# Kernel optimization log

Measured on AMD Instinct MI355X. Metric: run time of the kernel, lower is better.

The kernel has to match this reference:

```python
import jax, jax.numpy as jnp
import numpy as np

N_NODES = 50000
N_EDGES = 800000
IN_FEATS = 64
HID_FEATS = 64


def setup_inputs() -> dict:
    key = jax.random.key(0)
    ks = jax.random.split(key, 5)
    x = jax.random.normal(ks[0], (N_NODES, IN_FEATS), dtype=jnp.float32)
    src = jax.random.randint(ks[1], (N_EDGES,), 0, N_NODES)
    dst = jax.random.randint(ks[2], (N_EDGES,), 0, N_NODES)
    # GraphConv parameters (Glorot-ish init, bias zeros as in dgl defaults)
    W1 = jax.random.normal(ks[3], (IN_FEATS, HID_FEATS), dtype=jnp.float32) / np.sqrt(IN_FEATS)
    b1 = jnp.zeros((HID_FEATS,), dtype=jnp.float32)
    W2 = jax.random.normal(ks[4], (HID_FEATS, IN_FEATS), dtype=jnp.float32) / np.sqrt(HID_FEATS)
    b2 = jnp.zeros((IN_FEATS,), dtype=jnp.float32)
    return {"x": x, "src": src, "dst": dst, "W1": W1, "b1": b1, "W2": W2, "b2": b2}


def _graph_conv(x, src, dst, W, b, n_nodes):
    """dgl GraphConv with norm='both': D_dst^{-1/2} A D_src^{-1/2} X W + b."""
    ones = jnp.ones((src.shape[0],), dtype=x.dtype)
    deg_out = jax.ops.segment_sum(ones, src, num_segments=n_nodes)
    deg_in = jax.ops.segment_sum(ones, dst, num_segments=n_nodes)
    norm_out = jnp.where(deg_out > 0, jax.lax.rsqrt(jnp.maximum(deg_out, 1.0)), 0.0)
    norm_in = jnp.where(deg_in > 0, jax.lax.rsqrt(jnp.maximum(deg_in, 1.0)), 0.0)
    h = x * norm_out[:, None]                                  # [N, F] scaled by src norm
    agg = jax.ops.segment_sum(h[src], dst, num_segments=n_nodes)  # gather over edges + scatter-add
    return (agg * norm_in[:, None]) @ W + b


def reference(x, src, dst, W1, b1, W2, b2):
    n, d = x.shape
    # dHdx: conv -> tanh -> conv
    y = jnp.tanh(_graph_conv(x, src, dst, W1, b1, n))
    y = _graph_conv(y, src, dst, W2, b2, n)
    # J = cat([I[d//2:], -I[:d//2]])  -> symplectic [[0, I], [-I, 0]]
    I = jnp.eye(d, dtype=x.dtype)
    J = jnp.concatenate([I[d // 2:], -I[: d // 2]], axis=0)
    # get_D is undefined in the source module; treated as zero dissipation term.
    return y @ J.T
```

## Files before the change

### kernel.cpp

```cpp
#include <hip/hip_runtime.h>
#include <hip/hip_bf16.h>
#include <math.h>

#define N_NODES 50000
#define N_EDGES 800000
#define F 64
#define NPAD 50048
#define NBLK ((N_NODES + 255) / 256)

#define P_HIST 256
#define CHUNK (N_EDGES / P_HIST)
#define WORDS8 12500
#define RBLK8 ((WORDS8 + 255) / 256)
#define RSPLIT 4
#define WR (WORDS8 / RSPLIT)
#define HBLK (P_HIST * RSPLIT)

#define TW 20
#define RV3BLK (WORDS8 / TW)
#define TS 260

#define LROW 36
#define LBLK ((N_NODES + 31) / 32)

typedef short short8 __attribute__((ext_vector_type(8)));
typedef float f32x4 __attribute__((ext_vector_type(4)));

__device__ inline unsigned short f2bf(float f) {
    unsigned u = __float_as_uint(f);
    unsigned r = (u + 0x7fffu + ((u >> 16) & 1u)) >> 16;
    return (unsigned short)r;
}
__device__ inline float bf2f(unsigned v) { return __uint_as_float(v << 16); }
__device__ inline float bf2f_hi(unsigned v) { return __uint_as_float(v & 0xffff0000u); }

__device__ inline unsigned wave_incl_scan(unsigned v, int lane) {
    #pragma unroll
    for (int d = 1; d < 64; d <<= 1) {
        unsigned u = __shfl_up(v, d, 64);
        if (lane >= d) v += u;
    }
    return v;
}


__global__ __launch_bounds__(256) void hist2_kernel(
    const int* __restrict__ src, const int* __restrict__ dst,
    unsigned* __restrict__ histd, unsigned* __restrict__ hists)
{
    __shared__ unsigned ldd[WR];
    __shared__ unsigned lsd[WR];
    int bid = blockIdx.x, t = threadIdx.x;
    int p = bid >> 2, r = bid & 3;
    int e0 = p * CHUNK;
    unsigned wbase = (unsigned)(r * WR);
    for (int i = t; i < WR; i += 256) { ldd[i] = 0; lsd[i] = 0; }
    __syncthreads();
    for (int i = t; i < CHUNK; i += 256) {
        int d = dst[e0 + i];
        int s = src[e0 + i];
        unsigned wd = ((unsigned)d >> 2) - wbase;
        unsigned ws = ((unsigned)s >> 2) - wbase;
        if (wd < WR) atomicAdd(&ldd[wd], 1u << ((d & 3) * 8));
        if (ws < WR) atomicAdd(&lsd[ws], 1u << ((s & 3) * 8));
    }
    __syncthreads();
    unsigned* outd = histd + (size_t)p * WORDS8 + r * WR;
    unsigned* outs = hists + (size_t)p * WORDS8 + r * WR;
    for (int i = t; i < WR; i += 256) { outd[i] = ldd[i]; outs[i] = lsd[i]; }
}

__global__ __launch_bounds__(256) void reduce_v3_kernel(
    unsigned* __restrict__ histd, const unsigned* __restrict__ hists,
    float* __restrict__ norm_in, float* __restrict__ norm_out,
    int* __restrict__ row_off, unsigned* __restrict__ wordsum)
{
    __shared__ unsigned lds[TW * TS];
    int t = threadIdx.x, b = blockIdx.x;
    int lane = t & 63, ww = t >> 6;
    int w0 = b * TW;

    {
        uint4* gp = (uint4*)(histd + (size_t)t * WORDS8 + w0);
        #pragma unroll
        for (int i = 0; i < TW / 4; ++i) {
            uint4 v = gp[i];
            lds[(i * 4 + 0) * TS + t] = v.x;
            lds[(i * 4 + 1) * TS + t] = v.y;
            lds[(i * 4 + 2) * TS + t] = v.z;
            lds[(i * 4 + 3) * TS + t] = v.w;
        }
    }
    __syncthreads();
    #pragma unroll
    for (int k = 0; k < TW / 4; ++k) {
        int lw = ww + k * 4;
        uint4 h = *(uint4*)(lds + lw * TS + 4 * lane);
        unsigned lsum = h.x + h.y + h.z + h.w;
        unsigned inc = lsum;
        #pragma unroll
        for (int d = 1; d < 64; d <<= 1) {
            unsigned u = __shfl_up(inc, d, 64);
            if (lane >= d) inc += u;
        }
        unsigned run = inc - lsum;
        uint4 o;
        o.x = run; run += h.x;
        o.y = run; run += h.y;
        o.z = run; run += h.z;
        o.w = run;
        *(uint4*)(lds + lw * TS + 4 * lane) = o;
        unsigned total = __shfl(inc, 63, 64);
        if (lane == 0) {
            int w = w0 + lw;
            unsigned d0 = total & 255u, d1 = (total >> 8) & 255u;
            unsigned d2 = (total >> 16) & 255u, d3 = total >> 24;
            norm_in[4 * w]     = d0 ? rsqrtf((float)d0) : 0.f;
            norm_in[4 * w + 1] = d1 ? rsqrtf((float)d1) : 0.f;
            norm_in[4 * w + 2] = d2 ? rsqrtf((float)d2) : 0.f;
            norm_in[4 * w + 3] = d3 ? rsqrtf((float)d3) : 0.f;
            int4 r;
            r.x = 0; r.y = (int)d0; r.z = (int)(d0 + d1); r.w = (int)(d0 + d1 + d2);
            *(int4*)(row_off + 4 * w) = r;
            wordsum[w] = d0 + d1 + d2 + d3;
        }
    }
    __syncthreads();
    {
        uint4* gp = (uint4*)(histd + (size_t)t * WORDS8 + w0);
        #pragma unroll
        for (int i = 0; i < TW / 4; ++i) {
            uint4 v;
            v.x = lds[(i * 4 + 0) * TS + t];
            v.y = lds[(i * 4 + 1) * TS + t];
            v.z = lds[(i * 4 + 2) * TS + t];
            v.w = lds[(i * 4 + 3) * TS + t];
            gp[i] = v;
        }
    }
    __syncthreads();

    {
        const uint4* gp = (const uint4*)(hists + (size_t)t * WORDS8 + w0);
        #pragma unroll
        for (int i = 0; i < TW / 4; ++i) {
            uint4 v = gp[i];
            lds[(i * 4 + 0) * TS + t] = v.x;
            lds[(i * 4 + 1) * TS + t] = v.y;
            lds[(i * 4 + 2) * TS + t] = v.z;
            lds[(i * 4 + 3) * TS + t] = v.w;
        }
    }
    __syncthreads();
    #pragma unroll
    for (int k = 0; k < TW / 4; ++k) {
        int lw = ww + k * 4;
        uint4 h = *(uint4*)(lds + lw * TS + 4 * lane);
        unsigned s = h.x + h.y + h.z + h.w;
        #pragma unroll
        for (int d = 1; d < 64; d <<= 1) s += __shfl_xor(s, d, 64);
        if (lane == 0) {
            int w = w0 + lw;
            unsigned t0 = s & 255u, t1 = (s >> 8) & 255u;
            unsigned t2 = (s >> 16) & 255u, t3 = s >> 24;
            norm_out[4 * w]     = t0 ? rsqrtf((float)t0) : 0.f;
            norm_out[4 * w + 1] = t1 ? rsqrtf((float)t1) : 0.f;
            norm_out[4 * w + 2] = t2 ? rsqrtf((float)t2) : 0.f;
            norm_out[4 * w + 3] = t3 ? rsqrtf((float)t3) : 0.f;
        }
    }
}

__global__ __launch_bounds__(256) void scanw_kernel(
    const unsigned* __restrict__ wordsum, int* __restrict__ row_off,
    unsigned* __restrict__ blockSums)
{
    __shared__ unsigned wsum[4];
    int t = threadIdx.x, b = blockIdx.x;
    int w = b * 256 + t;
    unsigned v = (w < WORDS8) ? wordsum[w] : 0u;
    int lane = t & 63, wid = t >> 6;
    unsigned inc = wave_incl_scan(v, lane);
    if (lane == 63) wsum[wid] = inc;
    __syncthreads();
    if (t == 0) {
        unsigned acc = 0;
        #pragma unroll
        for (int q = 0; q < 4; ++q) { unsigned x = wsum[q]; wsum[q] = acc; acc += x; }
    }
    __syncthreads();
    unsigned excl = inc - v + wsum[wid];
    if (w < WORDS8) {
        int4 r = *(int4*)(row_off + 4 * w);
        r.x += (int)excl; r.y += (int)excl; r.z += (int)excl; r.w += (int)excl;
        *(int4*)(row_off + 4 * w) = r;
    }
    if (t == 255) blockSums[b] = excl + v;
}

__global__ __launch_bounds__(256) void scan_fin_kernel(
    const unsigned* __restrict__ blockSums, int* __restrict__ row_off)
{
    __shared__ unsigned off_s;
    int t = threadIdx.x, b = blockIdx.x;
    if (t < 64) {
        unsigned v = (t < b) ? blockSums[t] : 0u;
        #pragma unroll
        for (int d = 1; d < 64; d <<= 1) v += __shfl_xor(v, d, 64);
        if (t == 0) off_s = v;
    }
    __syncthreads();
    int off = (int)off_s;
    int w = b * 256 + t;
    if (w < WORDS8) {
        int4 r = *(int4*)(row_off + 4 * w);
        r.x += off; r.y += off; r.z += off; r.w += off;
        *(int4*)(row_off + 4 * w) = r;
    }
    if (w == 0) row_off[N_NODES] = N_EDGES;
}

__global__ __launch_bounds__(256) void scatter2_kernel(
    const int* __restrict__ src, const int* __restrict__ dst,
    const int* __restrict__ row_off, const unsigned* __restrict__ histd,
    int* __restrict__ csr_src)
{
    __shared__ unsigned rk[WR];
    __shared__ unsigned pf[WR];
    int bid = blockIdx.x, t = threadIdx.x;
    int p = bid >> 2, r = bid & 3;
    int e0 = p * CHUNK;
    unsigned wbase = (unsigned)(r * WR);
    const unsigned* pref = histd + (size_t)p * WORDS8 + r * WR;
    for (int i = t; i < WR; i += 256) { rk[i] = 0; pf[i] = pref[i]; }
    __syncthreads();
    for (int i = t; i < CHUNK; i += 256) {
        int d = dst[e0 + i];
        int s = src[e0 + i];
        unsigned wd = ((unsigned)d >> 2) - wbase;
        if (wd < WR) {
            int sh = (d & 3) * 8;
            unsigned old = atomicAdd(&rk[wd], 1u << sh);
            unsigned rank = (old >> sh) & 255u;
            unsigned pre  = (pf[wd] >> sh) & 255u;
            csr_src[row_off[d] + (int)(pre + rank)] = s;
        }
    }
}


__global__ __launch_bounds__(256) void degrees_kernel(
    const int* __restrict__ src, const int* __restrict__ dst,
    unsigned* __restrict__ deg_out_u, unsigned* __restrict__ deg_in_u)
{
    int e = blockIdx.x * 256 + threadIdx.x;
    if (e < N_EDGES) {
        atomicAdd(&deg_out_u[src[e]], 1u);
        atomicAdd(&deg_in_u[dst[e]], 1u);
    }
}

__global__ __launch_bounds__(256) void fb_scan_a_kernel(
    const unsigned* __restrict__ deg_in_u, const unsigned* __restrict__ deg_out_u,
    float* __restrict__ norm_out, float* __restrict__ norm_in,
    int* __restrict__ row_off, unsigned* __restrict__ blockSums)
{
    __shared__ unsigned wsum[4];
    int t = threadIdx.x, b = blockIdx.x;
    int idx = b * 256 + t;
    unsigned v = 0, dout = 0;
    if (idx < N_NODES) { v = deg_in_u[idx]; dout = deg_out_u[idx]; }
    int lane = t & 63, wid = t >> 6;
    unsigned inc = wave_incl_scan(v, lane);
    if (lane == 63) wsum[wid] = inc;
    __syncthreads();
    if (t == 0) {
        unsigned acc = 0;
        #pragma unroll
        for (int q = 0; q < 4; ++q) { unsigned x = wsum[q]; wsum[q] = acc; acc += x; }
    }
    __syncthreads();
    unsigned excl = inc - v + wsum[wid];
    if (idx < N_NODES) {
        row_off[idx] = (int)excl;
        norm_in[idx]  = v    ? rsqrtf((float)v)    : 0.f;
        norm_out[idx] = dout ? rsqrtf((float)dout) : 0.f;
    }
    if (t == 255) blockSums[b] = excl + v;
}

__global__ __launch_bounds__(256) void fb_scan_b_kernel(
    const unsigned* __restrict__ blockSums, unsigned* __restrict__ blockOff, int cnt)
{
    __shared__ unsigned wsum[4];
    int t = threadIdx.x;
    unsigned v = (t < cnt) ? blockSums[t] : 0u;
    int lane = t & 63, wid = t >> 6;
    unsigned inc = wave_incl_scan(v, lane);
    if (lane == 63) wsum[wid] = inc;
    __syncthreads();
    if (t == 0) {
        unsigned acc = 0;
        #pragma unroll
        for (int q = 0; q < 4; ++q) { unsigned x = wsum[q]; wsum[q] = acc; acc += x; }
    }
    __syncthreads();
    if (t < cnt) blockOff[t] = inc - v + wsum[wid];
}

__global__ __launch_bounds__(256) void fb_scan_c_kernel(
    const unsigned* __restrict__ blockOff, int* __restrict__ row_off,
    unsigned* __restrict__ cursor)
{
    int idx = blockIdx.x * 256 + threadIdx.x;
    if (idx < N_NODES) {
        int v = row_off[idx] + (int)blockOff[blockIdx.x];
        row_off[idx] = v;
        cursor[idx] = (unsigned)v;
    }
    if (idx == 0) row_off[N_NODES] = N_EDGES;
}

__global__ __launch_bounds__(256) void fb_csr_fill_kernel(
    const int* __restrict__ src, const int* __restrict__ dst,
    unsigned* __restrict__ cursor, int* __restrict__ csr_src)
{
    int e = blockIdx.x * 256 + threadIdx.x;
    if (e < N_EDGES) {
        unsigned p = atomicAdd(&cursor[dst[e]], 1u);
        csr_src[p] = src[e];
    }
}


__global__ __launch_bounds__(256) void prescale_kernel(
    const float* __restrict__ x, const float* __restrict__ norm_out,
    unsigned* __restrict__ xb)
{
    int t = blockIdx.x * 256 + threadIdx.x;
    if (t < N_NODES * 32) {
        int n = t >> 5;
        float w = norm_out[n];
        float2 v = ((const float2*)x)[t];
        xb[t] = (unsigned)f2bf(v.x * w) | ((unsigned)f2bf(v.y * w) << 16);
    }
}

__device__ inline void block_agg32(
    const unsigned* __restrict__ tab, const float* __restrict__ norm_in,
    const int* __restrict__ row_off, const int* __restrict__ csr_src,
    int nb, unsigned* lds)
{
    int tid = threadIdx.x;
    int wid = tid >> 6, lane = tid & 63;
    int g = lane >> 3, lp = lane & 7;
    int m = wid * 8 + g;
    int n = nb + m;
    float a0 = 0.f, a1 = 0.f, a2 = 0.f, a3 = 0.f;
    float a4 = 0.f, a5 = 0.f, a6 = 0.f, a7 = 0.f;
    float w = 0.f;
    if (n < N_NODES) {
        int beg = row_off[n];
        int end = row_off[n + 1];
        w = norm_in[n];
        int e = beg;
        for (; e + 3 < end; e += 4) {
            int s0 = csr_src[e], s1 = csr_src[e + 1];
            int s2 = csr_src[e + 2], s3 = csr_src[e + 3];
            uint4 v0 = *(const uint4*)(tab + (size_t)s0 * 32 + lp * 4);
            uint4 v1 = *(const uint4*)(tab + (size_t)s1 * 32 + lp * 4);
            uint4 v2 = *(const uint4*)(tab + (size_t)s2 * 32 + lp * 4);
            uint4 v3 = *(const uint4*)(tab + (size_t)s3 * 32 + lp * 4);
            a0 += bf2f(v0.x & 0xffffu); a1 += bf2f_hi(v0.x);
            a2 += bf2f(v0.y & 0xffffu); a3 += bf2f_hi(v0.y);
            a4 += bf2f(v0.z & 0xffffu); a5 += bf2f_hi(v0.z);
            a6 += bf2f(v0.w & 0xffffu); a7 += bf2f_hi(v0.w);
            a0 += bf2f(v1.x & 0xffffu); a1 += bf2f_hi(v1.x);
            a2 += bf2f(v1.y & 0xffffu); a3 += bf2f_hi(v1.y);
            a4 += bf2f(v1.z & 0xffffu); a5 += bf2f_hi(v1.z);
            a6 += bf2f(v1.w & 0xffffu); a7 += bf2f_hi(v1.w);
            a0 += bf2f(v2.x & 0xffffu); a1 += bf2f_hi(v2.x);
            a2 += bf2f(v2.y & 0xffffu); a3 += bf2f_hi(v2.y);
            a4 += bf2f(v2.z & 0xffffu); a5 += bf2f_hi(v2.z);
            a6 += bf2f(v2.w & 0xffffu); a7 += bf2f_hi(v2.w);
            a0 += bf2f(v3.x & 0xffffu); a1 += bf2f_hi(v3.x);
            a2 += bf2f(v3.y & 0xffffu); a3 += bf2f_hi(v3.y);
            a4 += bf2f(v3.z & 0xffffu); a5 += bf2f_hi(v3.z);
            a6 += bf2f(v3.w & 0xffffu); a7 += bf2f_hi(v3.w);
        }
        for (; e < end; ++e) {
            int s0 = csr_src[e];
            uint4 v0 = *(const uint4*)(tab + (size_t)s0 * 32 + lp * 4);
            a0 += bf2f(v0.x & 0xffffu); a1 += bf2f_hi(v0.x);
            a2 += bf2f(v0.y & 0xffffu); a3 += bf2f_hi(v0.y);
            a4 += bf2f(v0.z & 0xffffu); a5 += bf2f_hi(v0.z);
            a6 += bf2f(v0.w & 0xffffu); a7 += bf2f_hi(v0.w);
        }
    }
    uint4 o;
    o.x = (unsigned)f2bf(a0 * w) | ((unsigned)f2bf(a1 * w) << 16);
    o.y = (unsigned)f2bf(a2 * w) | ((unsigned)f2bf(a3 * w) << 16);
    o.z = (unsigned)f2bf(a4 * w) | ((unsigned)f2bf(a5 * w) << 16);
    o.w = (unsigned)f2bf(a6 * w) | ((unsigned)f2bf(a7 * w) << 16);
    *(uint4*)(lds + m * LROW + lp * 4) = o;
}

__global__ __launch_bounds__(256) void layer1_fused_kernel(
    const unsigned* __restrict__ tab, const float* __restrict__ norm_in,
    const float* __restrict__ norm_out, const int* __restrict__ row_off,
    const int* __restrict__ csr_src, const float* __restrict__ Wm,
    const float* __restrict__ bias, unsigned short* __restrict__ hb)
{
    __shared__ unsigned lds[32 * LROW];
    int tid = threadIdx.x;
    int wid = tid >> 6, lane = tid & 63;
    int q = lane >> 4, lp16 = lane & 15;
    int nb = blockIdx.x * 32;

    short8 bfrag[2];
    #pragma unroll
    for (int kt = 0; kt < 2; ++kt)
        #pragma unroll
        for (int j = 0; j < 8; ++j)
            bfrag[kt][j] = (short)f2bf(Wm[(kt * 32 + q * 8 + j) * F + wid * 16 + lp16]);

    block_agg32(tab, norm_in, row_off, csr_src, nb, lds);
    __syncthreads();

    int nn = wid * 16 + lp16;
    float bv = bias[nn];
    #pragma unroll
    for (int rg = 0; rg < 2; ++rg) {
        short8 afrag[2];
        #pragma unroll
        for (int kt = 0; kt < 2; ++kt)
            afrag[kt] = *(const short8*)(lds + (rg * 16 + lp16) * LROW + kt * 16 + q * 4);
        f32x4 acc = (f32x4){0.f, 0.f, 0.f, 0.f};
        #pragma unroll
        for (int kt = 0; kt < 2; ++kt)
            acc = __builtin_amdgcn_mfma_f32_16x16x32_bf16(afrag[kt], bfrag[kt], acc, 0, 0, 0);
        #pragma unroll
        for (int r = 0; r < 4; ++r) {
            int row = nb + rg * 16 + q * 4 + r;
            if (row < N_NODES) {
                float z = tanhf(acc[r] + bv) * norm_out[row];
                hb[(size_t)row * F + nn] = f2bf(z);
            }
        }
    }
}

__global__ __launch_bounds__(256) void layer2_fused_kernel(
    const unsigned* __restrict__ tab, const float* __restrict__ norm_in,
    const int* __restrict__ row_off, const int* __restrict__ csr_src,
    const float* __restrict__ Wm, const float* __restrict__ bias,
    float* __restrict__ out)
{
    __shared__ unsigned lds[32 * LROW];
    int tid = threadIdx.x;
    int wid = tid >> 6, lane = tid & 63;
    int q = lane >> 4, lp16 = lane & 15;
    int nb = blockIdx.x * 32;

    short8 bfrag[2];
    #pragma unroll
    for (int kt = 0; kt < 2; ++kt)
        #pragma unroll
        for (int j = 0; j < 8; ++j)
            bfrag[kt][j] = (short)f2bf(Wm[(kt * 32 + q * 8 + j) * F + wid * 16 + lp16]);

    block_agg32(tab, norm_in, row_off, csr_src, nb, lds);
    __syncthreads();

    int nn = wid * 16 + lp16;
    float bv = bias[nn];
    int oc = (nn + 32) & 63;
    float sgn = (nn < 32) ? -1.f : 1.f;
    #pragma unroll
    for (int rg = 0; rg < 2; ++rg) {
        short8 afrag[2];
        #pragma unroll
        for (int kt = 0; kt < 2; ++kt)
            afrag[kt] = *(const short8*)(lds + (rg * 16 + lp16) * LROW + kt * 16 + q * 4);
        f32x4 acc = (f32x4){0.f, 0.f, 0.f, 0.f};
        #pragma unroll
        for (int kt = 0; kt < 2; ++kt)
            acc = __builtin_amdgcn_mfma_f32_16x16x32_bf16(afrag[kt], bfrag[kt], acc, 0, 0, 0);
        #pragma unroll
        for (int r = 0; r < 4; ++r) {
            int row = nb + rg * 16 + q * 4 + r;
            if (row < N_NODES) {
                float z = acc[r] + bv;
                out[(size_t)row * F + oc] = sgn * z;
            }
        }
    }
}

extern "C" void kernel_launch(void* const* d_in, const int* in_sizes, int n_in,
                              void* d_out, int out_size, void* d_ws, size_t ws_size,
                              hipStream_t stream) {
    const float* x   = (const float*)d_in[0];
    const int*   src = (const int*)d_in[1];
    const int*   dst = (const int*)d_in[2];
    const float* W1  = (const float*)d_in[3];
    const float* b1  = (const float*)d_in[4];
    const float* W2  = (const float*)d_in[5];
    const float* b2  = (const float*)d_in[6];
    float* out = (float*)d_out;

    unsigned* ws = (unsigned*)d_ws;
    float*    norm_out = (float*)ws;
    float*    norm_in  = (float*)(ws + NPAD);
    int*      row_off  = (int*)(ws + 2 * NPAD);
    int*      csr_src  = (int*)(ws + 3 * NPAD);
    unsigned* xb       = ws + 3 * NPAD + N_EDGES;
    unsigned* hbu      = xb + (size_t)NPAD * 32;
    unsigned* blockSums= hbu + (size_t)NPAD * 32;
    unsigned* blockOff = blockSums + 256;
    unsigned* wordsum  = blockOff + 256;
    unsigned* tail     = wordsum + WORDS8;
    unsigned* histd = tail;
    unsigned* hists = histd + (size_t)P_HIST * WORDS8;
    size_t need_new = ((size_t)(tail - ws) + 2 * (size_t)P_HIST * WORDS8) * 4;

    if (ws_size >= need_new) {
        hist2_kernel<<<HBLK, 256, 0, stream>>>(src, dst, histd, hists);
        reduce_v3_kernel<<<RV3BLK, 256, 0, stream>>>(histd, hists, norm_in, norm_out, row_off, wordsum);
        scanw_kernel<<<RBLK8, 256, 0, stream>>>(wordsum, row_off, blockSums);
        scan_fin_kernel<<<RBLK8, 256, 0, stream>>>(blockSums, row_off);
        scatter2_kernel<<<HBLK, 256, 0, stream>>>(src, dst, row_off, histd, csr_src);
    } else {
        unsigned* deg_out_u = tail;
        unsigned* deg_in_u  = tail + NPAD;
        unsigned* cursor    = tail + 2 * NPAD;
        hipMemsetAsync(deg_out_u, 0, 2 * NPAD * sizeof(unsigned), stream);
        degrees_kernel<<<(N_EDGES + 255) / 256, 256, 0, stream>>>(src, dst, deg_out_u, deg_in_u);
        fb_scan_a_kernel<<<NBLK, 256, 0, stream>>>(deg_in_u, deg_out_u, norm_out, norm_in, row_off, blockSums);
        fb_scan_b_kernel<<<1, 256, 0, stream>>>(blockSums, blockOff, NBLK);
        fb_scan_c_kernel<<<NBLK, 256, 0, stream>>>(blockOff, row_off, cursor);
        fb_csr_fill_kernel<<<(N_EDGES + 255) / 256, 256, 0, stream>>>(src, dst, cursor, csr_src);
    }

    prescale_kernel<<<(N_NODES * 32 + 255) / 256, 256, 0, stream>>>(x, norm_out, xb);
    layer1_fused_kernel<<<LBLK, 256, 0, stream>>>(
        xb, norm_in, norm_out, row_off, csr_src, W1, b1, (unsigned short*)hbu);

    layer2_fused_kernel<<<LBLK, 256, 0, stream>>>(
        hbu, norm_in, row_off, csr_src, W2, b2, out);
}
```

Measured before the change: 165.2 us.

## Sort nodes by in-degree to balance aggregation work across waves

Adds a counting sort that builds a node permutation grouped by in-degree (histogram, scan, scatter kernels). The fused layer kernels then process nodes in permuted order, so the 8-lane groups in each wave have similar edge counts. This targets divergence and load imbalance in the gather loop. It costs three extra launches, and output writes become scattered by row. The hist/scatter block-to-partition mapping is also swapped so concurrently running blocks share the same edge chunk, and the weight fragment load moves after the aggregation.

```diff
diff --git a/kernel.cpp b/kernel.cpp
--- a/kernel.cpp
+++ b/kernel.cpp
@@ -20,6 +20,9 @@
 #define RV3BLK (WORDS8 / TW)
 #define TS 260
 
+#define DBINS 64
+#define PHW (DBINS * NBLK)
+
 #define LROW 36
 #define LBLK ((N_NODES + 31) / 32)
 
@@ -51,7 +54,7 @@
     __shared__ unsigned ldd[WR];
     __shared__ unsigned lsd[WR];
     int bid = blockIdx.x, t = threadIdx.x;
-    int p = bid >> 2, r = bid & 3;
+    int p = bid & 255, r = bid >> 8;
     int e0 = p * CHUNK;
     unsigned wbase = (unsigned)(r * WR);
     for (int i = t; i < WR; i += 256) { ldd[i] = 0; lsd[i] = 0; }
@@ -228,7 +231,7 @@
     __shared__ unsigned rk[WR];
     __shared__ unsigned pf[WR];
     int bid = blockIdx.x, t = threadIdx.x;
-    int p = bid >> 2, r = bid & 3;
+    int p = bid & 255, r = bid >> 8;
     int e0 = p * CHUNK;
     unsigned wbase = (unsigned)(r * WR);
     const unsigned* pref = histd + (size_t)p * WORDS8 + r * WR;
@@ -249,6 +252,71 @@
 }
 
 
+__global__ __launch_bounds__(256) void perm_hist_kernel(
+    const int* __restrict__ row_off, unsigned* __restrict__ permh)
+{
+    __shared__ unsigned cnt[DBINS];
+    int t = threadIdx.x, b = blockIdx.x;
+    if (t < DBINS) cnt[t] = 0;
+    __syncthreads();
+    int n = b * 256 + t;
+    if (n < N_NODES) {
+        int deg = row_off[n + 1] - row_off[n];
+        int bin = deg < DBINS ? deg : (DBINS - 1);
+        atomicAdd(&cnt[bin], 1u);
+    }
+    __syncthreads();
+    if (t < DBINS) permh[t * NBLK + b] = cnt[t];
+}
+
+__global__ __launch_bounds__(256) void perm_scan_kernel(unsigned* __restrict__ permh)
+{
+    __shared__ unsigned c[PHW];
+    __shared__ unsigned binOff[DBINS];
+    int t = threadIdx.x;
+    for (int i = t; i < PHW; i += 256) c[i] = permh[i];
+    __syncthreads();
+    unsigned tot = 0;
+    if (t < DBINS) {
+        unsigned run = 0;
+        int base = t * NBLK;
+        for (int b = 0; b < NBLK; ++b) {
+            unsigned v = c[base + b];
+            c[base + b] = run;
+            run += v;
+        }
+        tot = run;
+    }
+    if (t < 64) {
+        unsigned inc = wave_incl_scan(tot, t);
+        binOff[t] = inc - tot;
+    }
+    __syncthreads();
+    for (int i = t; i < PHW; i += 256) {
+        int bin = i / NBLK;
+        permh[i] = c[i] + binOff[bin];
+    }
+}
+
+__global__ __launch_bounds__(256) void perm_scatter_kernel(
+    const int* __restrict__ row_off, const unsigned* __restrict__ permh,
+    int* __restrict__ perm)
+{
+    __shared__ unsigned base[DBINS];
+    __shared__ unsigned cur[DBINS];
+    int t = threadIdx.x, b = blockIdx.x;
+    if (t < DBINS) { base[t] = permh[t * NBLK + b]; cur[t] = 0; }
+    __syncthreads();
+    int n = b * 256 + t;
+    if (n < N_NODES) {
+        int deg = row_off[n + 1] - row_off[n];
+        int bin = deg < DBINS ? deg : (DBINS - 1);
+        unsigned rk = atomicAdd(&cur[bin], 1u);
+        perm[base[bin] + rk] = n;
+    }
+}
+
+
 __global__ __launch_bounds__(256) void degrees_kernel(
     const int* __restrict__ src, const int* __restrict__ dst,
     unsigned* __restrict__ deg_out_u, unsigned* __restrict__ deg_in_u)
@@ -310,13 +378,14 @@
 
 __global__ __launch_bounds__(256) void fb_scan_c_kernel(
     const unsigned* __restrict__ blockOff, int* __restrict__ row_off,
-    unsigned* __restrict__ cursor)
+    unsigned* __restrict__ cursor, int* __restrict__ perm)
 {
     int idx = blockIdx.x * 256 + threadIdx.x;
     if (idx < N_NODES) {
         int v = row_off[idx] + (int)blockOff[blockIdx.x];
         row_off[idx] = v;
         cursor[idx] = (unsigned)v;
+        perm[idx] = idx;
     }
     if (idx == 0) row_off[N_NODES] = N_EDGES;
 }
@@ -349,17 +418,18 @@
 __device__ inline void block_agg32(
     const unsigned* __restrict__ tab, const float* __restrict__ norm_in,
     const int* __restrict__ row_off, const int* __restrict__ csr_src,
-    int nb, unsigned* lds)
+    const int* __restrict__ perm, int nb, unsigned* lds)
 {
     int tid = threadIdx.x;
     int wid = tid >> 6, lane = tid & 63;
     int g = lane >> 3, lp = lane & 7;
     int m = wid * 8 + g;
-    int n = nb + m;
+    int idx = nb + m;
     float a0 = 0.f, a1 = 0.f, a2 = 0.f, a3 = 0.f;
     float a4 = 0.f, a5 = 0.f, a6 = 0.f, a7 = 0.f;
     float w = 0.f;
-    if (n < N_NODES) {
+    if (idx < N_NODES) {
+        int n = perm[idx];
         int beg = row_off[n];
         int end = row_off[n + 1];
         w = norm_in[n];
@@ -408,8 +478,9 @@
 __global__ __launch_bounds__(256) void layer1_fused_kernel(
     const unsigned* __restrict__ tab, const float* __restrict__ norm_in,
     const float* __restrict__ norm_out, const int* __restrict__ row_off,
-    const int* __restrict__ csr_src, const float* __restrict__ Wm,
-    const float* __restrict__ bias, unsigned short* __restrict__ hb)
+    const int* __restrict__ csr_src, const int* __restrict__ perm,
+    const float* __restrict__ Wm, const float* __restrict__ bias,
+    unsigned short* __restrict__ hb)
 {
     __shared__ unsigned lds[32 * LROW];
     int tid = threadIdx.x;
@@ -417,6 +488,8 @@
     int q = lane >> 4, lp16 = lane & 15;
     int nb = blockIdx.x * 32;
 
+    block_agg32(tab, norm_in, row_off, csr_src, perm, nb, lds);
+
     short8 bfrag[2];
     #pragma unroll
     for (int kt = 0; kt < 2; ++kt)
@@ -424,7 +497,6 @@
         for (int j = 0; j < 8; ++j)
             bfrag[kt][j] = (short)f2bf(Wm[(kt * 32 + q * 8 + j) * F + wid * 16 + lp16]);
 
-    block_agg32(tab, norm_in, row_off, csr_src, nb, lds);
     __syncthreads();
 
     int nn = wid * 16 + lp16;
@@ -439,10 +511,12 @@
         #pragma unroll
         for (int kt = 0; kt < 2; ++kt)
             acc = __builtin_amdgcn_mfma_f32_16x16x32_bf16(afrag[kt], bfrag[kt], acc, 0, 0, 0);
+        int base = nb + rg * 16 + q * 4;
         #pragma unroll
         for (int r = 0; r < 4; ++r) {
-            int row = nb + rg * 16 + q * 4 + r;
-            if (row < N_NODES) {
+            int idx = base + r;
+            if (idx < N_NODES) {
+                int row = perm[idx];
                 float z = tanhf(acc[r] + bv) * norm_out[row];
                 hb[(size_t)row * F + nn] = f2bf(z);
             }
@@ -453,8 +527,8 @@
 __global__ __launch_bounds__(256) void layer2_fused_kernel(
     const unsigned* __restrict__ tab, const float* __restrict__ norm_in,
     const int* __restrict__ row_off, const int* __restrict__ csr_src,
-    const float* __restrict__ Wm, const float* __restrict__ bias,
-    float* __restrict__ out)
+    const int* __restrict__ perm, const float* __restrict__ Wm,
+    const float* __restrict__ bias, float* __restrict__ out)
 {
     __shared__ unsigned lds[32 * LROW];
     int tid = threadIdx.x;
@@ -462,6 +536,8 @@
     int q = lane >> 4, lp16 = lane & 15;
     int nb = blockIdx.x * 32;
 
+    block_agg32(tab, norm_in, row_off, csr_src, perm, nb, lds);
+
     short8 bfrag[2];
     #pragma unroll
     for (int kt = 0; kt < 2; ++kt)
@@ -469,7 +545,6 @@
         for (int j = 0; j < 8; ++j)
             bfrag[kt][j] = (short)f2bf(Wm[(kt * 32 + q * 8 + j) * F + wid * 16 + lp16]);
 
-    block_agg32(tab, norm_in, row_off, csr_src, nb, lds);
     __syncthreads();
 
     int nn = wid * 16 + lp16;
@@ -486,10 +561,12 @@
         #pragma unroll
         for (int kt = 0; kt < 2; ++kt)
             acc = __builtin_amdgcn_mfma_f32_16x16x32_bf16(afrag[kt], bfrag[kt], acc, 0, 0, 0);
+        int base = nb + rg * 16 + q * 4;
         #pragma unroll
         for (int r = 0; r < 4; ++r) {
-            int row = nb + rg * 16 + q * 4 + r;
-            if (row < N_NODES) {
+            int idx = base + r;
+            if (idx < N_NODES) {
+                int row = perm[idx];
                 float z = acc[r] + bv;
                 out[(size_t)row * F + oc] = sgn * z;
             }
@@ -519,7 +596,9 @@
     unsigned* blockSums= hbu + (size_t)NPAD * 32;
     unsigned* blockOff = blockSums + 256;
     unsigned* wordsum  = blockOff + 256;
-    unsigned* tail     = wordsum + WORDS8;
+    int*      perm     = (int*)(wordsum + WORDS8);
+    unsigned* permh    = (unsigned*)perm + NPAD;
+    unsigned* tail     = permh + PHW;
     unsigned* histd = tail;
     unsigned* hists = histd + (size_t)P_HIST * WORDS8;
     size_t need_new = ((size_t)(tail - ws) + 2 * (size_t)P_HIST * WORDS8) * 4;
@@ -530,6 +609,9 @@
         scanw_kernel<<<RBLK8, 256, 0, stream>>>(wordsum, row_off, blockSums);
         scan_fin_kernel<<<RBLK8, 256, 0, stream>>>(blockSums, row_off);
         scatter2_kernel<<<HBLK, 256, 0, stream>>>(src, dst, row_off, histd, csr_src);
+        perm_hist_kernel<<<NBLK, 256, 0, stream>>>(row_off, permh);
+        perm_scan_kernel<<<1, 256, 0, stream>>>(permh);
+        perm_scatter_kernel<<<NBLK, 256, 0, stream>>>(row_off, permh, perm);
     } else {
         unsigned* deg_out_u = tail;
         unsigned* deg_in_u  = tail + NPAD;
@@ -538,14 +620,14 @@
         degrees_kernel<<<(N_EDGES + 255) / 256, 256, 0, stream>>>(src, dst, deg_out_u, deg_in_u);
         fb_scan_a_kernel<<<NBLK, 256, 0, stream>>>(deg_in_u, deg_out_u, norm_out, norm_in, row_off, blockSums);
         fb_scan_b_kernel<<<1, 256, 0, stream>>>(blockSums, blockOff, NBLK);
-        fb_scan_c_kernel<<<NBLK, 256, 0, stream>>>(blockOff, row_off, cursor);
+        fb_scan_c_kernel<<<NBLK, 256, 0, stream>>>(blockOff, row_off, cursor, perm);
         fb_csr_fill_kernel<<<(N_EDGES + 255) / 256, 256, 0, stream>>>(src, dst, cursor, csr_src);
     }
 
     prescale_kernel<<<(N_NODES * 32 + 255) / 256, 256, 0, stream>>>(x, norm_out, xb);
     layer1_fused_kernel<<<LBLK, 256, 0, stream>>>(
-        xb, norm_in, norm_out, row_off, csr_src, W1, b1, (unsigned short*)hbu);
+        xb, norm_in, norm_out, row_off, csr_src, perm, W1, b1, (unsigned short*)hbu);
 
     layer2_fused_kernel<<<LBLK, 256, 0, stream>>>(
-        hbu, norm_in, row_off, csr_src, W2, b2, out);
-}
+        hbu, norm_in, row_off, csr_src, perm, W2, b2, out);
+}
```

After: 176.6 us. 6.9% more time.
